# Kernel tuning notes

Measured on AMD Instinct MI355X. Metric: run time of the kernel, lower is better.

Reference implementation:

```python
import jax, jax.numpy as jnp
import numpy as np

IN_CH = 512
HID = 1024
N_HEADS = 16
HEAD_DIM = HID // N_HEADS  # 64
BSZ = 1024
LN_EPS = 1e-5


def setup_inputs() -> dict:
    key = jax.random.key(0)
    ks = jax.random.split(key, 8)
    kvb_out = N_HEADS * (2 * HEAD_DIM + 1)
    return {
        "x": jax.random.normal(ks[0], (BSZ, IN_CH), dtype=jnp.float32),
        "W": jax.random.normal(ks[1], (BSZ, N_HEADS * HEAD_DIM * HEAD_DIM), dtype=jnp.float32) * 0.02,
        "w_in": jax.random.normal(ks[2], (HID, IN_CH), dtype=jnp.float32) * (1.0 / np.sqrt(IN_CH)),
        "b_in": jnp.zeros((HID,), dtype=jnp.float32),
        "gamma": jnp.ones((HID,), dtype=jnp.float32),
        "beta": jnp.zeros((HID,), dtype=jnp.float32),
        "w_kvb": jax.random.normal(ks[3], (kvb_out, HID), dtype=jnp.float32) * (1.0 / np.sqrt(HID)),
        "b_kvb": jnp.zeros((kvb_out,), dtype=jnp.float32),
    }


def reference(x, W, w_in, b_in, gamma, beta, w_kvb, b_kvb):
    bsz = x.shape[0]
    # input_proj + LayerNorm
    h = x @ w_in.T + b_in  # [B, HID]
    mu = jnp.mean(h, axis=-1, keepdims=True)
    var = jnp.mean((h - mu) ** 2, axis=-1, keepdims=True)
    h = (h - mu) * jax.lax.rsqrt(var + LN_EPS) * gamma + beta
    # kvb_net
    out = h @ w_kvb.T + b_kvb  # [B, H*(2d+1)]
    out = out.reshape(bsz, N_HEADS, 2 * HEAD_DIM + 1)
    ks_ = out[..., :HEAD_DIM]                    # [B, H, d]
    vs = jnp.tanh(out[..., HEAD_DIM:2 * HEAD_DIM])  # [B, H, d]
    lrs = jax.nn.sigmoid(out[..., 2 * HEAD_DIM:])   # [B, H, 1]
    # Oja removal: ks -= W^T v per head
    W_t = W.reshape(bsz, N_HEADS, HEAD_DIM, HEAD_DIM)
    ks_remove = jnp.einsum("bhij,bhi->bhj", W_t, vs)
    ks_ = ks_ - ks_remove
    ks_ = jax.nn.softmax(ks_, axis=-1) * lrs     # [B, H, d]
    # outer product v k^T per head
    dW = jnp.einsum("bhi,bhj->bhij", vs, ks_)    # [B, H, d, d]
    return dW.reshape(bsz, -1)
```

## Files before the change

### kernel.cpp

```cpp
#include <hip/hip_runtime.h>
#include <hip/hip_bf16.h>
#include <math.h>

#define IN_CH 512
#define HID   1024
#define NH    16
#define HD    64
#define BSZ   1024
#define KVB   2064
#define NPAD  2112
#define LN_EPS 1e-5f

typedef _Float16 f16x8 __attribute__((ext_vector_type(8)));
typedef float f32x4  __attribute__((ext_vector_type(4)));
typedef unsigned short u16;

__device__ inline void split16(float f, u16& hi, u16& lo) {
    _Float16 h = (_Float16)f;
    _Float16 l = (_Float16)(f - (float)h);
    hi = __builtin_bit_cast(u16, h);
    lo = __builtin_bit_cast(u16, l);
}
__device__ inline u16 f2h(float f) {
    _Float16 h = (_Float16)f;
    return __builtin_bit_cast(u16, h);
}

__device__ inline void gload16(const void* g, void* l) {
    __builtin_amdgcn_global_load_lds(
        (const __attribute__((address_space(1))) unsigned int*)g,
        (__attribute__((address_space(3))) unsigned int*)l, 16, 0, 0);
}

#define QX (BSZ * IN_CH / 4)
#define QW (HID * IN_CH / 4)
#define QK (NPAD * HID / 4)
#define QKVALID (KVB * HID / 4)
#define TOTQ (QX + QW + QK)

__global__ __launch_bounds__(256) void cvt_all(const float* __restrict__ x,
                                               const float* __restrict__ w_in,
                                               const float* __restrict__ w_kvb,
                                               u16* __restrict__ xh, u16* __restrict__ xl,
                                               u16* __restrict__ wih,
                                               u16* __restrict__ wkh) {
    long q = (long)blockIdx.x * 256 + threadIdx.x;
    if (q < QX) {
        float4 v = ((const float4*)x)[q];
        float f[4] = {v.x, v.y, v.z, v.w};
        ushort4 hh4, ll4;
        u16 hb[4], lb[4];
        #pragma unroll
        for (int j = 0; j < 4; ++j) split16(f[j], hb[j], lb[j]);
        hh4.x = hb[0]; hh4.y = hb[1]; hh4.z = hb[2]; hh4.w = hb[3];
        ll4.x = lb[0]; ll4.y = lb[1]; ll4.z = lb[2]; ll4.w = lb[3];
        ((ushort4*)xh)[q] = hh4;
        ((ushort4*)xl)[q] = ll4;
    } else if (q < QX + QW) {
        long lq = q - QX;
        float4 v = ((const float4*)w_in)[lq];
        ushort4 hh4;
        hh4.x = f2h(v.x); hh4.y = f2h(v.y); hh4.z = f2h(v.z); hh4.w = f2h(v.w);
        ((ushort4*)wih)[lq] = hh4;
    } else {
        long lq = q - QX - QW;
        float4 v = (lq < QKVALID) ? ((const float4*)w_kvb)[lq]
                                  : make_float4(0.f, 0.f, 0.f, 0.f);
        ushort4 hh4;
        hh4.x = f2h(v.x); hh4.y = f2h(v.y); hh4.z = f2h(v.z); hh4.w = f2h(v.w);
        ((ushort4*)wkh)[lq] = hh4;
    }
}

template<int BM, int BN, int KK, bool SWZ>
__global__ __launch_bounds__(256) void gemm_f16(const u16* __restrict__ Ah_g,
                                                const u16* __restrict__ Al_g,
                                                const u16* __restrict__ Bh_g,
                                                const float* __restrict__ bias,
                                                float* __restrict__ C,
                                                int N, int ldc) {
    constexpr int WM = BM / 2, WN = BN / 2, MF = WM / 16, NF = WN / 16;
    constexpr int UA = BM / 8;
    constexpr int UB = BN / 8;
    constexpr int U  = 2 * UA + UB;
    __shared__ __align__(16) u16 Ah[2][BM][64];
    __shared__ __align__(16) u16 Al[2][BM][64];
    __shared__ __align__(16) u16 Bh[2][BN][64];

    const int t = threadIdx.x, lane = t & 63, wid = t >> 6;
    const int wm = wid >> 1, wn = wid & 1;

    int mt, nt;
    if (SWZ) {
        int bid = blockIdx.x;
        int nwg = gridDim.x;
        int w = (bid & 7) * (nwg >> 3) + (bid >> 3);
        mt = w & (BSZ / BM - 1);
        nt = w / (BSZ / BM);
    } else {
        nt = blockIdx.x; mt = blockIdx.y;
    }
    const int m0 = mt * BM, n0 = nt * BN;

    const int seg = (lane & 7) ^ (lane >> 3);
    const int r8  = lane >> 3;

    f32x4 acc[MF][NF] = {};

    auto stage = [&](int buf, int k0) {
        #pragma unroll
        for (int it = 0; it < U / 4; ++it) {
            int u = it * 4 + wid;
            if (u < UA) {
                int row = u * 8 + r8;
                gload16(Ah_g + (size_t)(m0 + row) * KK + k0 + seg * 8,
                        &Ah[buf][u * 8][0]);
            } else if (u < 2 * UA) {
                int uu = u - UA;
                int row = uu * 8 + r8;
                gload16(Al_g + (size_t)(m0 + row) * KK + k0 + seg * 8,
                        &Al[buf][uu * 8][0]);
            } else {
                int bu = u - 2 * UA;
                int row = bu * 8 + r8;
                gload16(Bh_g + (size_t)(n0 + row) * KK + k0 + seg * 8,
                        &Bh[buf][bu * 8][0]);
            }
        }
    };

    constexpr int KT = KK / 64;
    stage(0, 0);
    __syncthreads();
    int buf = 0;
    for (int kt = 0; kt < KT; ++kt) {
        if (kt + 1 < KT) stage(buf ^ 1, (kt + 1) * 64);

        f16x8 ah[2][MF], al[2][MF], bh[2][NF];
        #pragma unroll
        for (int s = 0; s < 2; ++s) {
            #pragma unroll
            for (int mf = 0; mf < MF; ++mf) {
                int r = wm * WM + mf * 16 + (lane & 15);
                int pc = ((s << 2) | (lane >> 4)) ^ (r & 7);
                ah[s][mf] = *(const f16x8*)&Ah[buf][r][pc * 8];
                al[s][mf] = *(const f16x8*)&Al[buf][r][pc * 8];
            }
            #pragma unroll
            for (int nf = 0; nf < NF; ++nf) {
                int r = wn * WN + nf * 16 + (lane & 15);
                int pc = ((s << 2) | (lane >> 4)) ^ (r & 7);
                bh[s][nf] = *(const f16x8*)&Bh[buf][r][pc * 8];
            }
        }
        #pragma unroll
        for (int s = 0; s < 2; ++s)
            #pragma unroll
            for (int mf = 0; mf < MF; ++mf)
                #pragma unroll
                for (int nf = 0; nf < NF; ++nf) {
                    acc[mf][nf] = __builtin_amdgcn_mfma_f32_16x16x32_f16(ah[s][mf], bh[s][nf], acc[mf][nf], 0, 0, 0);
                    acc[mf][nf] = __builtin_amdgcn_mfma_f32_16x16x32_f16(al[s][mf], bh[s][nf], acc[mf][nf], 0, 0, 0);
                }
        __syncthreads();
        buf ^= 1;
    }

    #pragma unroll
    for (int mf = 0; mf < MF; ++mf)
        #pragma unroll
        for (int nf = 0; nf < NF; ++nf) {
            int col = n0 + wn * WN + nf * 16 + (lane & 15);
            if (col < N) {
                float bb = bias[col];
                #pragma unroll
                for (int r = 0; r < 4; ++r) {
                    int row = m0 + wm * WM + mf * 16 + ((lane >> 4) << 2) + r;
                    C[(size_t)row * ldc + col] = acc[mf][nf][r] + bb;
                }
            }
        }
}

__global__ __launch_bounds__(256) void ln_rows(const float* __restrict__ h,
                                               const float* __restrict__ gamma,
                                               const float* __restrict__ beta,
                                               u16* __restrict__ hh,
                                               u16* __restrict__ hl) {
    const int row = blockIdx.x;
    const int t   = threadIdx.x;
    const float* hr = h + (size_t)row * HID;

    float4 v = *(const float4*)(hr + t * 4);
    float s  = v.x + v.y + v.z + v.w;
    float sq = v.x * v.x + v.y * v.y + v.z * v.z + v.w * v.w;

    #pragma unroll
    for (int off = 1; off < 64; off <<= 1) {
        s  += __shfl_xor(s, off);
        sq += __shfl_xor(sq, off);
    }
    __shared__ float red[8];
    const int wid = t >> 6;
    if ((t & 63) == 0) { red[wid] = s; red[4 + wid] = sq; }
    __syncthreads();
    s  = red[0] + red[1] + red[2] + red[3];
    sq = red[4] + red[5] + red[6] + red[7];

    const float mu  = s * (1.f / HID);
    const float var = sq * (1.f / HID) - mu * mu;
    const float inv = rsqrtf(var + LN_EPS);

    float4 g  = *(const float4*)(gamma + t * 4);
    float4 be = *(const float4*)(beta + t * 4);
    float o[4];
    o[0] = (v.x - mu) * inv * g.x + be.x;
    o[1] = (v.y - mu) * inv * g.y + be.y;
    o[2] = (v.z - mu) * inv * g.z + be.z;
    o[3] = (v.w - mu) * inv * g.w + be.w;

    ushort4 uh, ul;
    u16 hb[4], lb[4];
    #pragma unroll
    for (int j = 0; j < 4; ++j) split16(o[j], hb[j], lb[j]);
    uh.x = hb[0]; uh.y = hb[1]; uh.z = hb[2]; uh.w = hb[3];
    ul.x = lb[0]; ul.y = lb[1]; ul.z = lb[2]; ul.w = lb[3];
    ((ushort4*)(hh + (size_t)row * HID))[t] = uh;
    ((ushort4*)(hl + (size_t)row * HID))[t] = ul;
}

__global__ __launch_bounds__(256) void oja_tail(const float* __restrict__ out2,
                                                const float* __restrict__ W,
                                                float* __restrict__ dW) {
    const int lane = threadIdx.x & 63;
    const int wid  = threadIdx.x >> 6;
    const int pair = blockIdx.x * 4 + wid;
    const int b    = pair >> 4;
    const int head = pair & 15;

    const float* orow = out2 + (size_t)b * KVB + head * (2 * HD + 1);

    const float kin   = orow[lane];
    const float vfull = tanhf(orow[64 + lane]);
    float t3 = 0.f;
    if (lane == 0) t3 = orow[128];
    const float lrl = __shfl(t3, 0);
    const float lr  = 1.f / (1.f + expf(-lrl));

    const int g   = lane >> 4;
    const int c16 = lane & 15;

    const f32x4* wbh = (const f32x4*)(W + (size_t)pair * (HD * HD));

    float rem[4] = {0.f, 0.f, 0.f, 0.f};
    #pragma unroll
    for (int tt = 0; tt < 16; ++tt) {
        const int i = 4 * tt + g;
        const float vsi = __shfl(vfull, i);
        f32x4 w4 = __builtin_nontemporal_load(wbh + i * 16 + c16);
        rem[0] = fmaf(w4[0], vsi, rem[0]);
        rem[1] = fmaf(w4[1], vsi, rem[1]);
        rem[2] = fmaf(w4[2], vsi, rem[2]);
        rem[3] = fmaf(w4[3], vsi, rem[3]);
    }
    #pragma unroll
    for (int q = 0; q < 4; ++q) {
        rem[q] += __shfl_xor(rem[q], 16);
        rem[q] += __shfl_xor(rem[q], 32);
    }

    float L[4];
    #pragma unroll
    for (int q = 0; q < 4; ++q)
        L[q] = __shfl(kin, 4 * c16 + q) - rem[q];

    float mx = fmaxf(fmaxf(L[0], L[1]), fmaxf(L[2], L[3]));
    #pragma unroll
    for (int off = 1; off < 16; off <<= 1)
        mx = fmaxf(mx, __shfl_xor(mx, off));

    float e[4], ssum = 0.f;
    #pragma unroll
    for (int q = 0; q < 4; ++q) { e[q] = expf(L[q] - mx); ssum += e[q]; }
    #pragma unroll
    for (int off = 1; off < 16; off <<= 1)
        ssum += __shfl_xor(ssum, off);

    const float scale = lr / ssum;
    float ks[4];
    #pragma unroll
    for (int q = 0; q < 4; ++q) ks[q] = e[q] * scale;

    f32x4* obh = (f32x4*)(dW + (size_t)pair * (HD * HD));
    #pragma unroll
    for (int tt = 0; tt < 16; ++tt) {
        const int i = 4 * tt + g;
        const float vsi = __shfl(vfull, i);
        f32x4 o;
        o[0] = vsi * ks[0]; o[1] = vsi * ks[1];
        o[2] = vsi * ks[2]; o[3] = vsi * ks[3];
        __builtin_nontemporal_store(o, obh + i * 16 + c16);
    }
}

extern "C" void kernel_launch(void* const* d_in, const int* in_sizes, int n_in,
                              void* d_out, int out_size, void* d_ws, size_t ws_size,
                              hipStream_t stream) {
    const float* x     = (const float*)d_in[0];
    const float* W     = (const float*)d_in[1];
    const float* w_in  = (const float*)d_in[2];
    const float* b_in  = (const float*)d_in[3];
    const float* gamma = (const float*)d_in[4];
    const float* beta  = (const float*)d_in[5];
    const float* w_kvb = (const float*)d_in[6];
    const float* b_kvb = (const float*)d_in[7];
    float* dW = (float*)d_out;

    char* p = (char*)d_ws;
    auto carve = [&](size_t bytes) { char* r = p; p += (bytes + 255) & ~(size_t)255; return r; };
    float* h    = (float*)carve((size_t)BSZ * HID * 4);
    float* out2 = (float*)carve((size_t)BSZ * KVB * 4);
    u16* xh  = (u16*)carve((size_t)BSZ * IN_CH * 2);
    u16* xl  = (u16*)carve((size_t)BSZ * IN_CH * 2);
    u16* wih = (u16*)carve((size_t)HID * IN_CH * 2);
    u16* hh  = (u16*)carve((size_t)BSZ * HID * 2);
    u16* hl  = (u16*)carve((size_t)BSZ * HID * 2);
    u16* wkh = (u16*)carve((size_t)NPAD * HID * 2);

    cvt_all<<<TOTQ / 256, 256, 0, stream>>>(x, w_in, w_kvb, xh, xl, wih, wkh);

    gemm_f16<32, 64, IN_CH, false><<<dim3(HID / 64, BSZ / 32), 256, 0, stream>>>(
        xh, xl, wih, b_in, h, HID, HID);

    ln_rows<<<BSZ, 256, 0, stream>>>(h, gamma, beta, hh, hl);

    gemm_f16<64, 64, HID, true><<<(NPAD / 64) * (BSZ / 64), 256, 0, stream>>>(
        hh, hl, wkh, b_kvb, out2, KVB, KVB);

    oja_tail<<<(BSZ * NH) / 4, 256, 0, stream>>>(out2, W, dW);
}
```

Baseline: 137.5 us.

## Fuse kvb GEMM and Oja tail into one persistent kernel with per-row-tile flags

Merges the second GEMM and the Oja tail into one 1024-block launch. The first 176 blocks each compute three 64x64 GEMM tiles with a smaller K-step of 32. They then bump a per-M-tile completion counter with atomics. Every block prefetches half of its W slice, spins until its M-tile's 33 column tiles are finished, and then runs the softmax/outer-product tail for one batch row (16 heads, four per wave). The goal is to overlap streaming the large W/dW arrays with the GEMM and to drop one launch. The cost is spin-waiting, reliance on all blocks being co-resident, and less GEMM parallelism with a shorter K tile.

Result: slower. 416.4 us (+202.9%).

```diff
diff --git a/kernel.cpp b/kernel.cpp
--- a/kernel.cpp
+++ b/kernel.cpp
@@ -10,6 +10,9 @@
 #define KVB   2064
 #define NPAD  2112
 #define LN_EPS 1e-5f
+
+#define NG    176
+#define POOL  1024
 
 typedef _Float16 f16x8 __attribute__((ext_vector_type(8)));
 typedef float f32x4  __attribute__((ext_vector_type(4)));
@@ -72,7 +75,7 @@
     }
 }
 
-template<int BM, int BN, int KK, bool SWZ>
+template<int BM, int BN, int KK>
 __global__ __launch_bounds__(256) void gemm_f16(const u16* __restrict__ Ah_g,
                                                 const u16* __restrict__ Al_g,
                                                 const u16* __restrict__ Bh_g,
@@ -81,26 +84,14 @@
                                                 int N, int ldc) {
     constexpr int WM = BM / 2, WN = BN / 2, MF = WM / 16, NF = WN / 16;
     constexpr int UA = BM / 8;
-    constexpr int UB = BN / 8;
-    constexpr int U  = 2 * UA + UB;
+    constexpr int U  = 2 * UA + BN / 8;
     __shared__ __align__(16) u16 Ah[2][BM][64];
     __shared__ __align__(16) u16 Al[2][BM][64];
     __shared__ __align__(16) u16 Bh[2][BN][64];
 
     const int t = threadIdx.x, lane = t & 63, wid = t >> 6;
     const int wm = wid >> 1, wn = wid & 1;
-
-    int mt, nt;
-    if (SWZ) {
-        int bid = blockIdx.x;
-        int nwg = gridDim.x;
-        int w = (bid & 7) * (nwg >> 3) + (bid >> 3);
-        mt = w & (BSZ / BM - 1);
-        nt = w / (BSZ / BM);
-    } else {
-        nt = blockIdx.x; mt = blockIdx.y;
-    }
-    const int m0 = mt * BM, n0 = nt * BN;
+    const int m0 = blockIdx.y * BM, n0 = blockIdx.x * BN;
 
     const int seg = (lane & 7) ^ (lane >> 3);
     const int r8  = lane >> 3;
@@ -229,17 +220,16 @@
     ((ushort4*)(hl + (size_t)row * HID))[t] = ul;
 }
 
-__global__ __launch_bounds__(256) void oja_tail(const float* __restrict__ out2,
-                                                const float* __restrict__ W,
-                                                float* __restrict__ dW) {
-    const int lane = threadIdx.x & 63;
-    const int wid  = threadIdx.x >> 6;
-    const int pair = blockIdx.x * 4 + wid;
-    const int b    = pair >> 4;
-    const int head = pair & 15;
-
-    const float* orow = out2 + (size_t)b * KVB + head * (2 * HD + 1);
-
+__global__ void zero_sync(unsigned* __restrict__ done) {
+    if (threadIdx.x < 16) done[threadIdx.x] = 0u;
+}
+
+template<int NPRE>
+__device__ __forceinline__ void tail_pair(const float* __restrict__ orow,
+                                          const float* __restrict__ Wb,
+                                          float* __restrict__ dWb,
+                                          const int lane,
+                                          const f32x4 (&pre)[8]) {
     const float kin   = orow[lane];
     const float vfull = tanhf(orow[64 + lane]);
     float t3 = 0.f;
@@ -249,15 +239,15 @@
 
     const int g   = lane >> 4;
     const int c16 = lane & 15;
-
-    const f32x4* wbh = (const f32x4*)(W + (size_t)pair * (HD * HD));
+    const f32x4* wbh = (const f32x4*)Wb;
 
     float rem[4] = {0.f, 0.f, 0.f, 0.f};
     #pragma unroll
     for (int tt = 0; tt < 16; ++tt) {
         const int i = 4 * tt + g;
         const float vsi = __shfl(vfull, i);
-        f32x4 w4 = __builtin_nontemporal_load(wbh + i * 16 + c16);
+        f32x4 w4 = (tt < NPRE) ? pre[tt]
+                               : __builtin_nontemporal_load(wbh + i * 16 + c16);
         rem[0] = fmaf(w4[0], vsi, rem[0]);
         rem[1] = fmaf(w4[1], vsi, rem[1]);
         rem[2] = fmaf(w4[2], vsi, rem[2]);
@@ -291,7 +281,7 @@
     #pragma unroll
     for (int q = 0; q < 4; ++q) ks[q] = e[q] * scale;
 
-    f32x4* obh = (f32x4*)(dW + (size_t)pair * (HD * HD));
+    f32x4* obh = (f32x4*)dWb;
     #pragma unroll
     for (int tt = 0; tt < 16; ++tt) {
         const int i = 4 * tt + g;
@@ -300,6 +290,138 @@
         o[0] = vsi * ks[0]; o[1] = vsi * ks[1];
         o[2] = vsi * ks[2]; o[3] = vsi * ks[3];
         __builtin_nontemporal_store(o, obh + i * 16 + c16);
+    }
+}
+
+__global__ __launch_bounds__(256, 4) void fused2(const u16* __restrict__ hh,
+                                                 const u16* __restrict__ hl,
+                                                 const u16* __restrict__ wkh,
+                                                 const float* __restrict__ b_kvb,
+                                                 float* __restrict__ out2,
+                                                 const float* __restrict__ W,
+                                                 float* __restrict__ dW,
+                                                 unsigned* __restrict__ done) {
+    __shared__ __align__(16) u16 Ah[2][64][32];
+    __shared__ __align__(16) u16 Al[2][64][32];
+    __shared__ __align__(16) u16 Bh[2][64][32];
+
+    const int t = threadIdx.x, lane = t & 63, wid = t >> 6;
+    const int bid = blockIdx.x;
+    const int wm = wid >> 1, wn = wid & 1;
+
+    if (bid < NG) {
+        #pragma unroll 1
+        for (int j = 0; j < 3; ++j) {
+            const int idx = bid + NG * j;
+            const int mt = idx / 33, ntl = idx % 33;
+            const int m0 = mt * 64, n0 = ntl * 64;
+
+            f32x4 acc[2][2] = {};
+
+            auto stage = [&](int buf, int k0) {
+                #pragma unroll
+                for (int it = 0; it < 3; ++it) {
+                    int u = it * 4 + wid;
+                    int row16 = lane >> 2;
+                    int seg = (lane & 3) ^ (row16 & 3);
+                    if (u < 4) {
+                        int row = u * 16 + row16;
+                        gload16(hh + (size_t)(m0 + row) * HID + k0 + seg * 8,
+                                &Ah[buf][u * 16][0]);
+                    } else if (u < 8) {
+                        int row = (u - 4) * 16 + row16;
+                        gload16(hl + (size_t)(m0 + row) * HID + k0 + seg * 8,
+                                &Al[buf][(u - 4) * 16][0]);
+                    } else {
+                        int row = (u - 8) * 16 + row16;
+                        gload16(wkh + (size_t)(n0 + row) * HID + k0 + seg * 8,
+                                &Bh[buf][(u - 8) * 16][0]);
+                    }
+                }
+            };
+
+            stage(0, 0);
+            __syncthreads();
+            int buf = 0;
+            for (int kt = 0; kt < 32; ++kt) {
+                if (kt + 1 < 32) stage(buf ^ 1, (kt + 1) * 32);
+
+                f16x8 a_h[2], a_l[2], b_h[2];
+                #pragma unroll
+                for (int mf = 0; mf < 2; ++mf) {
+                    int r = wm * 32 + mf * 16 + (lane & 15);
+                    int pc = (lane >> 4) ^ (r & 3);
+                    a_h[mf] = *(const f16x8*)&Ah[buf][r][pc * 8];
+                    a_l[mf] = *(const f16x8*)&Al[buf][r][pc * 8];
+                }
+                #pragma unroll
+                for (int nf = 0; nf < 2; ++nf) {
+                    int r = wn * 32 + nf * 16 + (lane & 15);
+                    int pc = (lane >> 4) ^ (r & 3);
+                    b_h[nf] = *(const f16x8*)&Bh[buf][r][pc * 8];
+                }
+                #pragma unroll
+                for (int mf = 0; mf < 2; ++mf)
+                    #pragma unroll
+                    for (int nf = 0; nf < 2; ++nf) {
+                        acc[mf][nf] = __builtin_amdgcn_mfma_f32_16x16x32_f16(a_h[mf], b_h[nf], acc[mf][nf], 0, 0, 0);
+                        acc[mf][nf] = __builtin_amdgcn_mfma_f32_16x16x32_f16(a_l[mf], b_h[nf], acc[mf][nf], 0, 0, 0);
+                    }
+                __syncthreads();
+                buf ^= 1;
+            }
+
+            #pragma unroll
+            for (int mf = 0; mf < 2; ++mf)
+                #pragma unroll
+                for (int nf = 0; nf < 2; ++nf) {
+                    int col = n0 + wn * 32 + nf * 16 + (lane & 15);
+                    if (col < KVB) {
+                        float bb = b_kvb[col];
+                        #pragma unroll
+                        for (int r = 0; r < 4; ++r) {
+                            int row = m0 + wm * 32 + mf * 16 + ((lane >> 4) << 2) + r;
+                            out2[(size_t)row * KVB + col] = acc[mf][nf][r] + bb;
+                        }
+                    }
+                }
+
+            __threadfence();
+            __syncthreads();
+            if (t == 0)
+                __hip_atomic_fetch_add(&done[mt], 1u, __ATOMIC_RELEASE,
+                                       __HIP_MEMORY_SCOPE_AGENT);
+        }
+    }
+
+    const int rank = (bid < NG) ? (POOL - NG + bid) : (bid - NG);
+    const int b    = rank;
+    const int mtw  = b >> 6;
+    const int head0 = wid * 4;
+    const int g = lane >> 4, c16 = lane & 15;
+
+    const float* Wb0  = W  + ((size_t)b * NH + head0) * (HD * HD);
+    float*       dWb0 = dW + ((size_t)b * NH + head0) * (HD * HD);
+    const float* orow0 = out2 + (size_t)b * KVB + head0 * (2 * HD + 1);
+
+    f32x4 pre[8];
+    #pragma unroll
+    for (int tt = 0; tt < 8; ++tt) {
+        int i = 4 * tt + g;
+        pre[tt] = __builtin_nontemporal_load((const f32x4*)Wb0 + i * 16 + c16);
+    }
+
+    while (__hip_atomic_load(&done[mtw], __ATOMIC_RELAXED,
+                             __HIP_MEMORY_SCOPE_AGENT) < 33u)
+        __builtin_amdgcn_s_sleep(8);
+    __threadfence();
+
+    tail_pair<8>(orow0, Wb0, dWb0, lane, pre);
+    #pragma unroll 1
+    for (int q = 1; q < 4; ++q) {
+        tail_pair<0>(orow0 + q * (2 * HD + 1),
+                     Wb0  + (size_t)q * HD * HD,
+                     dWb0 + (size_t)q * HD * HD, lane, pre);
     }
 }
 
@@ -326,16 +448,16 @@
     u16* hh  = (u16*)carve((size_t)BSZ * HID * 2);
     u16* hl  = (u16*)carve((size_t)BSZ * HID * 2);
     u16* wkh = (u16*)carve((size_t)NPAD * HID * 2);
+    unsigned* done = (unsigned*)carve(64);
 
     cvt_all<<<TOTQ / 256, 256, 0, stream>>>(x, w_in, w_kvb, xh, xl, wih, wkh);
 
-    gemm_f16<32, 64, IN_CH, false><<<dim3(HID / 64, BSZ / 32), 256, 0, stream>>>(
+    zero_sync<<<1, 64, 0, stream>>>(done);
+
+    gemm_f16<32, 64, IN_CH><<<dim3(HID / 64, BSZ / 32), 256, 0, stream>>>(
         xh, xl, wih, b_in, h, HID, HID);
 
     ln_rows<<<BSZ, 256, 0, stream>>>(h, gamma, beta, hh, hl);
 
-    gemm_f16<64, 64, HID, true><<<(NPAD / 64) * (BSZ / 64), 256, 0, stream>>>(
-        hh, hl, wkh, b_kvb, out2, KVB, KVB);
-
-    oja_tail<<<(BSZ * NH) / 4, 256, 0, stream>>>(out2, W, dW);
-}
+    fused2<<<POOL, 256, 0, stream>>>(hh, hl, wkh, b_kvb, out2, W, dW, done);
+}
```

## Drop hi/lo fp16 split for activations, move w_kvb conversion into LN kernel

Applied to the files above, without the earlier changes.

Both GEMMs now use a single fp16 copy of the activations instead of the high/low split pair. This halves the MFMA count and the A-side LDS and global traffic, and removes the xl/hl buffers. The w_kvb fp16 conversion moves from the first convert kernel into extra blocks of the LayerNorm launch, and oja_tail now issues all its W loads before the tanh/sigmoid work so they overlap. The cost is lower precision in the activations, which may raise error relative to the fp32 reference.

Result: faster. 128.8 us (-6.3%).

```diff
diff --git a/kernel.cpp b/kernel.cpp
--- a/kernel.cpp
+++ b/kernel.cpp
@@ -15,12 +15,6 @@
 typedef float f32x4  __attribute__((ext_vector_type(4)));
 typedef unsigned short u16;
 
-__device__ inline void split16(float f, u16& hi, u16& lo) {
-    _Float16 h = (_Float16)f;
-    _Float16 l = (_Float16)(f - (float)h);
-    hi = __builtin_bit_cast(u16, h);
-    lo = __builtin_bit_cast(u16, l);
-}
 __device__ inline u16 f2h(float f) {
     _Float16 h = (_Float16)f;
     return __builtin_bit_cast(u16, h);
@@ -36,55 +30,31 @@
 #define QW (HID * IN_CH / 4)
 #define QK (NPAD * HID / 4)
 #define QKVALID (KVB * HID / 4)
-#define TOTQ (QX + QW + QK)
-
-__global__ __launch_bounds__(256) void cvt_all(const float* __restrict__ x,
-                                               const float* __restrict__ w_in,
-                                               const float* __restrict__ w_kvb,
-                                               u16* __restrict__ xh, u16* __restrict__ xl,
-                                               u16* __restrict__ wih,
-                                               u16* __restrict__ wkh) {
+
+__global__ __launch_bounds__(256) void cvt_xw(const float* __restrict__ x,
+                                              const float* __restrict__ w_in,
+                                              u16* __restrict__ xh,
+                                              u16* __restrict__ wih) {
     long q = (long)blockIdx.x * 256 + threadIdx.x;
-    if (q < QX) {
-        float4 v = ((const float4*)x)[q];
-        float f[4] = {v.x, v.y, v.z, v.w};
-        ushort4 hh4, ll4;
-        u16 hb[4], lb[4];
-        #pragma unroll
-        for (int j = 0; j < 4; ++j) split16(f[j], hb[j], lb[j]);
-        hh4.x = hb[0]; hh4.y = hb[1]; hh4.z = hb[2]; hh4.w = hb[3];
-        ll4.x = lb[0]; ll4.y = lb[1]; ll4.z = lb[2]; ll4.w = lb[3];
-        ((ushort4*)xh)[q] = hh4;
-        ((ushort4*)xl)[q] = ll4;
-    } else if (q < QX + QW) {
-        long lq = q - QX;
-        float4 v = ((const float4*)w_in)[lq];
-        ushort4 hh4;
-        hh4.x = f2h(v.x); hh4.y = f2h(v.y); hh4.z = f2h(v.z); hh4.w = f2h(v.w);
-        ((ushort4*)wih)[lq] = hh4;
-    } else {
-        long lq = q - QX - QW;
-        float4 v = (lq < QKVALID) ? ((const float4*)w_kvb)[lq]
-                                  : make_float4(0.f, 0.f, 0.f, 0.f);
-        ushort4 hh4;
-        hh4.x = f2h(v.x); hh4.y = f2h(v.y); hh4.z = f2h(v.z); hh4.w = f2h(v.w);
-        ((ushort4*)wkh)[lq] = hh4;
-    }
+    const float* src; u16* dst; long lq;
+    if (q < QX) { src = x;    dst = xh;  lq = q; }
+    else        { src = w_in; dst = wih; lq = q - QX; }
+    float4 v = ((const float4*)src)[lq];
+    ushort4 hh4;
+    hh4.x = f2h(v.x); hh4.y = f2h(v.y); hh4.z = f2h(v.z); hh4.w = f2h(v.w);
+    ((ushort4*)dst)[lq] = hh4;
 }
 
 template<int BM, int BN, int KK, bool SWZ>
-__global__ __launch_bounds__(256) void gemm_f16(const u16* __restrict__ Ah_g,
-                                                const u16* __restrict__ Al_g,
-                                                const u16* __restrict__ Bh_g,
-                                                const float* __restrict__ bias,
-                                                float* __restrict__ C,
-                                                int N, int ldc) {
+__global__ __launch_bounds__(256) void gemm_f16x(const u16* __restrict__ Ah_g,
+                                                 const u16* __restrict__ Bh_g,
+                                                 const float* __restrict__ bias,
+                                                 float* __restrict__ C,
+                                                 int N, int ldc) {
     constexpr int WM = BM / 2, WN = BN / 2, MF = WM / 16, NF = WN / 16;
     constexpr int UA = BM / 8;
-    constexpr int UB = BN / 8;
-    constexpr int U  = 2 * UA + UB;
+    constexpr int U  = UA + BN / 8;
     __shared__ __align__(16) u16 Ah[2][BM][64];
-    __shared__ __align__(16) u16 Al[2][BM][64];
     __shared__ __align__(16) u16 Bh[2][BN][64];
 
     const int t = threadIdx.x, lane = t & 63, wid = t >> 6;
@@ -92,9 +62,8 @@
 
     int mt, nt;
     if (SWZ) {
-        int bid = blockIdx.x;
-        int nwg = gridDim.x;
-        int w = (bid & 7) * (nwg >> 3) + (bid >> 3);
+        const int bid = blockIdx.x, nwg = gridDim.x;
+        const int w = (bid & 7) * (nwg >> 3) + (bid >> 3);
         mt = w & (BSZ / BM - 1);
         nt = w / (BSZ / BM);
     } else {
@@ -115,13 +84,8 @@
                 int row = u * 8 + r8;
                 gload16(Ah_g + (size_t)(m0 + row) * KK + k0 + seg * 8,
                         &Ah[buf][u * 8][0]);
-            } else if (u < 2 * UA) {
-                int uu = u - UA;
-                int row = uu * 8 + r8;
-                gload16(Al_g + (size_t)(m0 + row) * KK + k0 + seg * 8,
-                        &Al[buf][uu * 8][0]);
             } else {
-                int bu = u - 2 * UA;
+                int bu = u - UA;
                 int row = bu * 8 + r8;
                 gload16(Bh_g + (size_t)(n0 + row) * KK + k0 + seg * 8,
                         &Bh[buf][bu * 8][0]);
@@ -136,7 +100,7 @@
     for (int kt = 0; kt < KT; ++kt) {
         if (kt + 1 < KT) stage(buf ^ 1, (kt + 1) * 64);
 
-        f16x8 ah[2][MF], al[2][MF], bh[2][NF];
+        f16x8 ah[2][MF], bh[2][NF];
         #pragma unroll
         for (int s = 0; s < 2; ++s) {
             #pragma unroll
@@ -144,7 +108,6 @@
                 int r = wm * WM + mf * 16 + (lane & 15);
                 int pc = ((s << 2) | (lane >> 4)) ^ (r & 7);
                 ah[s][mf] = *(const f16x8*)&Ah[buf][r][pc * 8];
-                al[s][mf] = *(const f16x8*)&Al[buf][r][pc * 8];
             }
             #pragma unroll
             for (int nf = 0; nf < NF; ++nf) {
@@ -158,10 +121,8 @@
             #pragma unroll
             for (int mf = 0; mf < MF; ++mf)
                 #pragma unroll
-                for (int nf = 0; nf < NF; ++nf) {
+                for (int nf = 0; nf < NF; ++nf)
                     acc[mf][nf] = __builtin_amdgcn_mfma_f32_16x16x32_f16(ah[s][mf], bh[s][nf], acc[mf][nf], 0, 0, 0);
-                    acc[mf][nf] = __builtin_amdgcn_mfma_f32_16x16x32_f16(al[s][mf], bh[s][nf], acc[mf][nf], 0, 0, 0);
-                }
         __syncthreads();
         buf ^= 1;
     }
@@ -182,13 +143,24 @@
         }
 }
 
-__global__ __launch_bounds__(256) void ln_rows(const float* __restrict__ h,
-                                               const float* __restrict__ gamma,
-                                               const float* __restrict__ beta,
-                                               u16* __restrict__ hh,
-                                               u16* __restrict__ hl) {
-    const int row = blockIdx.x;
+__global__ __launch_bounds__(256) void ln_mix(const float* __restrict__ h,
+                                              const float* __restrict__ gamma,
+                                              const float* __restrict__ beta,
+                                              u16* __restrict__ hh,
+                                              const float* __restrict__ w_kvb,
+                                              u16* __restrict__ wkh) {
+    const int bid = blockIdx.x;
     const int t   = threadIdx.x;
+    if (bid >= BSZ) {
+        long lq = (long)(bid - BSZ) * 256 + t;
+        float4 v = (lq < QKVALID) ? ((const float4*)w_kvb)[lq]
+                                  : make_float4(0.f, 0.f, 0.f, 0.f);
+        ushort4 hh4;
+        hh4.x = f2h(v.x); hh4.y = f2h(v.y); hh4.z = f2h(v.z); hh4.w = f2h(v.w);
+        ((ushort4*)wkh)[lq] = hh4;
+        return;
+    }
+    const int row = bid;
     const float* hr = h + (size_t)row * HID;
 
     float4 v = *(const float4*)(hr + t * 4);
@@ -219,14 +191,9 @@
     o[2] = (v.z - mu) * inv * g.z + be.z;
     o[3] = (v.w - mu) * inv * g.w + be.w;
 
-    ushort4 uh, ul;
-    u16 hb[4], lb[4];
-    #pragma unroll
-    for (int j = 0; j < 4; ++j) split16(o[j], hb[j], lb[j]);
-    uh.x = hb[0]; uh.y = hb[1]; uh.z = hb[2]; uh.w = hb[3];
-    ul.x = lb[0]; ul.y = lb[1]; ul.z = lb[2]; ul.w = lb[3];
+    ushort4 uh;
+    uh.x = f2h(o[0]); uh.y = f2h(o[1]); uh.z = f2h(o[2]); uh.w = f2h(o[3]);
     ((ushort4*)(hh + (size_t)row * HID))[t] = uh;
-    ((ushort4*)(hl + (size_t)row * HID))[t] = ul;
 }
 
 __global__ __launch_bounds__(256) void oja_tail(const float* __restrict__ out2,
@@ -238,8 +205,16 @@
     const int b    = pair >> 4;
     const int head = pair & 15;
 
+    const int g   = lane >> 4;
+    const int c16 = lane & 15;
+
+    const f32x4* wbh = (const f32x4*)(W + (size_t)pair * (HD * HD));
+    f32x4 wv[16];
+    #pragma unroll
+    for (int tt = 0; tt < 16; ++tt)
+        wv[tt] = __builtin_nontemporal_load(wbh + (4 * tt + g) * 16 + c16);
+
     const float* orow = out2 + (size_t)b * KVB + head * (2 * HD + 1);
-
     const float kin   = orow[lane];
     const float vfull = tanhf(orow[64 + lane]);
     float t3 = 0.f;
@@ -247,21 +222,14 @@
     const float lrl = __shfl(t3, 0);
     const float lr  = 1.f / (1.f + expf(-lrl));
 
-    const int g   = lane >> 4;
-    const int c16 = lane & 15;
-
-    const f32x4* wbh = (const f32x4*)(W + (size_t)pair * (HD * HD));
-
     float rem[4] = {0.f, 0.f, 0.f, 0.f};
     #pragma unroll
     for (int tt = 0; tt < 16; ++tt) {
-        const int i = 4 * tt + g;
-        const float vsi = __shfl(vfull, i);
-        f32x4 w4 = __builtin_nontemporal_load(wbh + i * 16 + c16);
-        rem[0] = fmaf(w4[0], vsi, rem[0]);
-        rem[1] = fmaf(w4[1], vsi, rem[1]);
-        rem[2] = fmaf(w4[2], vsi, rem[2]);
-        rem[3] = fmaf(w4[3], vsi, rem[3]);
+        const float vsi = __shfl(vfull, 4 * tt + g);
+        rem[0] = fmaf(wv[tt][0], vsi, rem[0]);
+        rem[1] = fmaf(wv[tt][1], vsi, rem[1]);
+        rem[2] = fmaf(wv[tt][2], vsi, rem[2]);
+        rem[3] = fmaf(wv[tt][3], vsi, rem[3]);
     }
     #pragma unroll
     for (int q = 0; q < 4; ++q) {
@@ -321,21 +289,19 @@
     float* h    = (float*)carve((size_t)BSZ * HID * 4);
     float* out2 = (float*)carve((size_t)BSZ * KVB * 4);
     u16* xh  = (u16*)carve((size_t)BSZ * IN_CH * 2);
-    u16* xl  = (u16*)carve((size_t)BSZ * IN_CH * 2);
     u16* wih = (u16*)carve((size_t)HID * IN_CH * 2);
     u16* hh  = (u16*)carve((size_t)BSZ * HID * 2);
-    u16* hl  = (u16*)carve((size_t)BSZ * HID * 2);
     u16* wkh = (u16*)carve((size_t)NPAD * HID * 2);
 
-    cvt_all<<<TOTQ / 256, 256, 0, stream>>>(x, w_in, w_kvb, xh, xl, wih, wkh);
-
-    gemm_f16<32, 64, IN_CH, false><<<dim3(HID / 64, BSZ / 32), 256, 0, stream>>>(
-        xh, xl, wih, b_in, h, HID, HID);
-
-    ln_rows<<<BSZ, 256, 0, stream>>>(h, gamma, beta, hh, hl);
-
-    gemm_f16<64, 64, HID, true><<<(NPAD / 64) * (BSZ / 64), 256, 0, stream>>>(
-        hh, hl, wkh, b_kvb, out2, KVB, KVB);
+    cvt_xw<<<(QX + QW) / 256, 256, 0, stream>>>(x, w_in, xh, wih);
+
+    gemm_f16x<32, 64, IN_CH, false><<<dim3(HID / 64, BSZ / 32), 256, 0, stream>>>(
+        xh, wih, b_in, h, HID, HID);
+
+    ln_mix<<<BSZ + QK / 256, 256, 0, stream>>>(h, gamma, beta, hh, w_kvb, wkh);
+
+    gemm_f16x<64, 64, HID, true><<<(NPAD / 64) * (BSZ / 64), 256, 0, stream>>>(
+        hh, wkh, b_kvb, out2, KVB, KVB);
 
     oja_tail<<<(BSZ * NH) / 4, 256, 0, stream>>>(out2, W, dW);
 }
```
